# Optimization experiments

Measured on AMD Instinct MI355X. Metric: run time of the kernel, lower is better.

## Reference

```python
import jax, jax.numpy as jnp
import numpy as np
import math

EMBED_DIM = 768
NUM_HEADS = 12
HEAD_DIM = EMBED_DIM // NUM_HEADS
R = 16
LORA_ALPHA = 16
SCALING = LORA_ALPHA / math.sqrt(R)  # 4.0
U = 1.0  # ramp_up_steps=0 -> u()=1.0


def lora_linear(x, W, b, A):
    # base F.linear + SingLoRA delta: delta_W = A @ A.T (symmetric)
    base = x @ W.T + b
    delta_W = A @ A.T  # [D, D]
    return base + (x @ delta_W.T) * (U * SCALING)


def setup_inputs() -> dict:
    key = jax.random.key(0)
    ks = jax.random.split(key, 16)
    B, S, D = 2, 2048, EMBED_DIM
    inv = 1.0 / math.sqrt(D)
    d = {
        'query': jax.random.normal(ks[0], (B, S, D), jnp.float32),
        'key': jax.random.normal(ks[1], (B, S, D), jnp.float32),
        'value': jax.random.normal(ks[2], (B, S, D), jnp.float32),
        'Wq': jax.random.normal(ks[3], (D, D), jnp.float32) * inv,
        'bq': jax.random.normal(ks[4], (D,), jnp.float32) * 0.01,
        'Aq': jax.random.normal(ks[5], (D, R), jnp.float32) * 0.01,
        'Wk': jax.random.normal(ks[6], (D, D), jnp.float32) * inv,
        'bk': jax.random.normal(ks[7], (D,), jnp.float32) * 0.01,
        'Ak': jax.random.normal(ks[8], (D, R), jnp.float32) * 0.01,
        'Wv': jax.random.normal(ks[9], (D, D), jnp.float32) * inv,
        'bv': jax.random.normal(ks[10], (D,), jnp.float32) * 0.01,
        'Av': jax.random.normal(ks[11], (D, R), jnp.float32) * 0.01,
        'Wo': jax.random.normal(ks[12], (D, D), jnp.float32) * inv,
        'bo': jax.random.normal(ks[13], (D,), jnp.float32) * 0.01,
    }
    return d


def reference(query, key, value, Wq, bq, Aq, Wk, bk, Ak, Wv, bv, Av, Wo, bo):
    B, S, D = query.shape
    H, hd = NUM_HEADS, HEAD_DIM
    q = lora_linear(query, Wq, bq, Aq)
    k = lora_linear(key, Wk, bk, Ak)
    v = lora_linear(value, Wv, bv, Av)
    # [B, S, D] -> [B, H, S, hd]
    q = q.reshape(B, S, H, hd).transpose(0, 2, 1, 3)
    k = k.reshape(B, S, H, hd).transpose(0, 2, 1, 3)
    v = v.reshape(B, S, H, hd).transpose(0, 2, 1, 3)
    scores = jnp.einsum('bhqd,bhkd->bhqk', q, k) / math.sqrt(hd)
    attn = jax.nn.softmax(scores, axis=-1)
    out = jnp.einsum('bhqk,bhkd->bhqd', attn, v)  # [B, H, S, hd]
    out = out.transpose(0, 2, 1, 3).reshape(B, S, D)
    out = out @ Wo.T + bo
    return out
```

## Files before the change

### kernel.cpp

```cpp
#include <hip/hip_runtime.h>
#include <math.h>
#include <stdint.h>

#define D 768
#define S 2048
#define B_ 2
#define NROWS 4096
#define H 12
#define HD 64
#define R_ 16

typedef _Float16 half_t;
typedef _Float16 half8 __attribute__((ext_vector_type(8)));
typedef _Float16 half4 __attribute__((ext_vector_type(4)));
typedef float floatx4 __attribute__((ext_vector_type(4)));

#define MFMA32(a, b, c) __builtin_amdgcn_mfma_f32_16x16x32_f16(a, b, c, 0, 0, 0)
#define EXP2F(x) __builtin_amdgcn_exp2f(x)

#define SWAIT(N) __builtin_amdgcn_s_waitcnt(0x0F70 | (N))
#define SBAR() __builtin_amdgcn_s_barrier()

__device__ __forceinline__ void gl_lds16(const void* gp, half_t* lp) {
  __builtin_amdgcn_global_load_lds(
      (const __attribute__((address_space(1))) void*)(gp),
      (__attribute__((address_space(3))) void*)(lp), 16, 0, 0);
}


__global__ __launch_bounds__(256) void prep_kernel(
    const float* __restrict__ q, const float* __restrict__ k,
    const float* __restrict__ v, half_t* __restrict__ xq,
    half_t* __restrict__ xk, half_t* __restrict__ xv,
    const float* __restrict__ Wq, const float* __restrict__ Aq,
    const float* __restrict__ Wk, const float* __restrict__ Ak,
    const float* __restrict__ Wv, const float* __restrict__ Av,
    const float* __restrict__ Wo, half_t* __restrict__ Mq,
    half_t* __restrict__ Mk, half_t* __restrict__ Mv,
    half_t* __restrict__ Mo) {
  const int bid = blockIdx.x;
  if (bid < 9216) {
    const int y = bid / 3072;
    const float* x = (y == 0) ? q : (y == 1) ? k : v;
    half_t* o = (y == 0) ? xq : (y == 1) ? xk : xv;
    int i = (bid - y * 3072) * 1024 + threadIdx.x * 4;
    float4 vv = *reinterpret_cast<const float4*>(x + i);
    half_t tmp[4] = {(half_t)vv.x, (half_t)vv.y, (half_t)vv.z, (half_t)vv.w};
    *reinterpret_cast<uint64_t*>(o + i) = *reinterpret_cast<uint64_t*>(tmp);
  } else {
    const int u = bid - 9216;
    const int y = u / 2304;
    const float* W = (y == 0) ? Wq : (y == 1) ? Wk : (y == 2) ? Wv : Wo;
    const float* A = (y == 0) ? Aq : (y == 1) ? Ak : (y == 2) ? Av : nullptr;
    half_t* M = (y == 0) ? Mq : (y == 1) ? Mk : (y == 2) ? Mv : Mo;
    int idx = (u - y * 2304) * 256 + threadIdx.x;
    int j = idx / D;
    int kk = idx - j * D;
    float acc = W[idx];
    if (A != nullptr) {
      float s = 0.f;
#pragma unroll
      for (int r = 0; r < R_; ++r) s += A[kk * R_ + r] * A[j * R_ + r];
      acc += 4.0f * s;
    }
    M[idx] = (half_t)acc;
  }
}

__global__ __launch_bounds__(256) void gemm_qkv_kernel(
    const half_t* __restrict__ x0, const half_t* __restrict__ x1,
    const half_t* __restrict__ x2, const half_t* __restrict__ m0,
    const half_t* __restrict__ m1, const half_t* __restrict__ m2,
    const float* __restrict__ b0, const float* __restrict__ b1,
    const float* __restrict__ b2, half_t* __restrict__ o0,
    half_t* __restrict__ o1, half_t* __restrict__ o2) {
  constexpr int AG = 8;
  constexpr int G = 16;
  constexpr int PB = G * 512;
  __shared__ __align__(16) half_t smem[3 * PB];

  int lin = blockIdx.x + 6 * (blockIdx.y + 32 * blockIdx.z);
  lin = (lin & 7) * 72 + (lin >> 3);
  const int z = lin / 192;
  const int rem = lin - z * 192;
  const int by = rem / 6;
  const int bx = rem - by * 6;

  const half_t* X = (z == 0) ? x0 : (z == 1) ? x1 : x2;
  const half_t* M = (z == 0) ? m0 : (z == 1) ? m1 : m2;
  const float* bias = (z == 0) ? b0 : (z == 1) ? b1 : b2;
  half_t* Out = (z == 0) ? o0 : (z == 1) ? o1 : o2;

  const int tid = threadIdx.x;
  const int lane = tid & 63;
  const int wv = tid >> 6;
  const int lr = lane & 15;
  const int lq = lane >> 4;
  const int row0 = by * 128;
  const int j0 = bx * 128;
  const int wr = wv >> 1;
  const int wc = wv & 1;

  floatx4 acc[4][4] = {};

#define GSTAGE(soff, k0)                                                      \
  do {                                                                        \
    _Pragma("unroll") for (int gi = 0; gi < 4; ++gi) {                        \
      int g = wv * 4 + gi;                                                    \
      if (g < AG) {                                                           \
        gl_lds16(X + (size_t)(row0 + g * 16 + lr) * D + (k0) + lq * 8,        \
                 smem + (soff) + g * 512);                                    \
      } else {                                                                \
        gl_lds16(M + (size_t)(j0 + (g - AG) * 16 + lr) * D + (k0) + lq * 8,   \
                 smem + (soff) + g * 512);                                    \
      }                                                                       \
    }                                                                         \
  } while (0)

  GSTAGE(0, 0);
  GSTAGE(PB, 32);
  SWAIT(4);
  SBAR();

  int co = 0, so = 2 * PB;
  for (int it = 0; it < D / 32; ++it) {
    if (it + 2 < D / 32) GSTAGE(so, (it + 2) * 32);
    const half_t* Ab = smem + co;
    const half_t* Bb = Ab + AG * 512;
    half8 af[4], bf[4];
#pragma unroll
    for (int t = 0; t < 4; ++t)
      af[t] = *reinterpret_cast<const half8*>(
          &Ab[((wr * 4 + t) * 64 + lane) * 8]);
#pragma unroll
    for (int u = 0; u < 4; ++u)
      bf[u] = *reinterpret_cast<const half8*>(
          &Bb[((wc * 4 + u) * 64 + lane) * 8]);
#pragma unroll
    for (int t = 0; t < 4; ++t)
#pragma unroll
      for (int u = 0; u < 4; ++u) acc[t][u] = MFMA32(af[t], bf[u], acc[t][u]);
    if (it + 2 < D / 32) SWAIT(4); else SWAIT(0);
    SBAR();
    co += PB; if (co == 3 * PB) co = 0;
    so += PB; if (so == 3 * PB) so = 0;
  }
#undef GSTAGE

  float bv[4];
#pragma unroll
  for (int u = 0; u < 4; ++u) bv[u] = bias[j0 + (wc * 4 + u) * 16 + lr];

  if (z == 2) {
    const int bb = row0 >> 11;
    const int kb0 = (row0 & 2047) >> 6;
#pragma unroll
    for (int t = 0; t < 4; ++t) {
#pragma unroll
      for (int u = 0; u < 4; ++u) {
        int gc = j0 + (wc * 4 + u) * 16 + lr;
        int hh = gc >> 6;
        int ud = (gc & 63) >> 4;
        half4 hv;
#pragma unroll
        for (int r = 0; r < 4; ++r) hv[r] = (half_t)(acc[t][u][r] + bv[u]);
        size_t addr = ((size_t)(bb * H + hh) * HD) * S +
                      (size_t)(kb0 + wr) * 4096 +
                      (ud * 2 + ((t >> 1) & 1)) * 512 + lane * 8 + (t & 1) * 4;
        *reinterpret_cast<half4*>(&Out[addr]) = hv;
      }
    }
    return;
  }

#pragma unroll
  for (int t = 0; t < 4; ++t) {
#pragma unroll
    for (int u = 0; u < 4; ++u) {
#pragma unroll
      for (int r = 0; r < 4; ++r) {
        int gr = row0 + (wr * 4 + t) * 16 + lq * 4 + r;
        int gc = j0 + (wc * 4 + u) * 16 + lr;
        Out[(size_t)gr * D + gc] = (half_t)(acc[t][u][r] + bv[u]);
      }
    }
  }
}

__global__ __launch_bounds__(256) void gemm_o_kernel(
    const half_t* __restrict__ Xh, const half_t* __restrict__ M,
    const float* __restrict__ bias, float* __restrict__ Out) {
  constexpr int AG = 8;
  constexpr int G = 16;
  constexpr int PB = G * 512;
  __shared__ __align__(16) half_t smem[3 * PB];

  int lin = blockIdx.x + 12 * blockIdx.y;
  lin = (lin & 7) * 96 + (lin >> 3);
  const int bx = lin % 12;
  const int byy = lin / 12;

  const int tid = threadIdx.x;
  const int lane = tid & 63;
  const int wv = tid >> 6;
  const int lr = lane & 15;
  const int lq = lane >> 4;
  const int row0 = byy * 64;
  const int j0 = bx * 64;
  const int wr = wv >> 1;
  const int wc = wv & 1;

  floatx4 acc[2][2] = {};

#define GSTAGE(soff, k0)                                                       \
  do {                                                                         \
    _Pragma("unroll") for (int gi = 0; gi < 4; ++gi) {                         \
      int g = wv * 4 + gi;                                                     \
      if (g < AG) {                                                            \
        int t = g >> 1, c = g & 1;                                             \
        gl_lds16(                                                              \
            Xh + (size_t)(row0 + t * 16 + lr) * D + (k0) + c * 32 + lq * 8,    \
            smem + (soff) + g * 512);                                          \
      } else {                                                                 \
        int g2 = g - AG;                                                       \
        int u = g2 >> 1, c = g2 & 1;                                           \
        gl_lds16(                                                              \
            M + (size_t)(j0 + u * 16 + lr) * D + (k0) + c * 32 + lq * 8,       \
            smem + (soff) + AG * 512 + g2 * 512);                              \
      }                                                                        \
    }                                                                          \
  } while (0)

  GSTAGE(0, 0);
  GSTAGE(PB, 64);
  SWAIT(4);
  SBAR();

  int co = 0, so = 2 * PB;
  for (int it = 0; it < D / 64; ++it) {
    if (it + 2 < D / 64) GSTAGE(so, (it + 2) * 64);
    const half_t* Ab = smem + co;
    const half_t* Bb = Ab + AG * 512;
#pragma unroll
    for (int c = 0; c < 2; ++c) {
      half8 af[2], bf[2];
#pragma unroll
      for (int t = 0; t < 2; ++t)
        af[t] = *reinterpret_cast<const half8*>(
            &Ab[(((wr * 2 + t) * 2 + c) * 64 + lane) * 8]);
#pragma unroll
      for (int u = 0; u < 2; ++u)
        bf[u] = *reinterpret_cast<const half8*>(
            &Bb[(((wc * 2 + u) * 2 + c) * 64 + lane) * 8]);
#pragma unroll
      for (int t = 0; t < 2; ++t)
#pragma unroll
        for (int u = 0; u < 2; ++u) acc[t][u] = MFMA32(af[t], bf[u], acc[t][u]);
    }
    if (it + 2 < D / 64) SWAIT(4); else SWAIT(0);
    SBAR();
    co += PB; if (co == 3 * PB) co = 0;
    so += PB; if (so == 3 * PB) so = 0;
  }
#undef GSTAGE

  float bv[2];
#pragma unroll
  for (int u = 0; u < 2; ++u) bv[u] = bias[j0 + (wc * 2 + u) * 16 + lr];
#pragma unroll
  for (int t = 0; t < 2; ++t) {
#pragma unroll
    for (int u = 0; u < 2; ++u) {
#pragma unroll
      for (int r = 0; r < 4; ++r) {
        int gr = row0 + (wr * 2 + t) * 16 + lq * 4 + r;
        int gc = j0 + (wc * 2 + u) * 16 + lr;
        Out[(size_t)gr * D + gc] = acc[t][u][r] + bv[u];
      }
    }
  }
}

__global__ __launch_bounds__(512, 6) void attn_mfma_kernel(
    const half_t* __restrict__ Qh, const half_t* __restrict__ Kh,
    const half_t* __restrict__ Vt2, half_t* __restrict__ Oh) {
  __shared__ __align__(16) half_t smem[24576];
  half_t* Ks = smem;
  half_t* Vs = smem + 12288;

  const int tid = threadIdx.x;
  const int lane = tid & 63;
  const int wv = tid >> 6;
  const int t_ = wv & 3;
  const int half_ = wv >> 2;
  const int lr = lane & 15;
  const int lq = lane >> 4;

  int lin = blockIdx.x + 32 * (blockIdx.y + 12 * blockIdx.z);
  lin = (lin & 7) * 96 + (lin >> 3);
  const int q0 = (lin & 31) * 64;
  const int hb = lin >> 5;
  const int h = hb % 12;
  const int b = hb / 12;

  const size_t base = (size_t)b * S * D + h * HD;
  const size_t vtbase = (size_t)(b * H + h) * HD * (size_t)S;
  const int qw = q0 + t_ * 16;

  const half_t qscale = (half_t)0.18033688f;
  half8 qf[2];
#pragma unroll
  for (int c = 0; c < 2; ++c) {
    half8 qv = *reinterpret_cast<const half8*>(
        &Qh[base + (size_t)(qw + lr) * D + c * 32 + lq * 8]);
#pragma unroll
    for (int j = 0; j < 8; ++j) qv[j] = qv[j] * qscale;
    qf[c] = qv;
  }

  half8 ones8;
#pragma unroll
  for (int j = 0; j < 8; ++j) ones8[j] = (half_t)1.0f;

  floatx4 o[4] = {};
  floatx4 ol = {};

#define STAGE(soff, kb)                                                        \
  do {                                                                         \
    _Pragma("unroll") for (int gi = 0; gi < 2; ++gi) {                         \
      int g = wv * 2 + gi;                                                     \
      if (g < 8) {                                                             \
        int u = g >> 1, c = g & 1;                                             \
        gl_lds16(                                                              \
            Kh + base + (size_t)((kb) + u * 16 + lr) * D + c * 32 + lq * 8,    \
            Ks + (soff) + g * 512);                                            \
      } else {                                                                 \
        int gv = g - 8;                                                        \
        gl_lds16(Vt2 + vtbase + (size_t)(kb)*64 + gv * 512 + lane * 8,         \
                 Vs + (soff) + gv * 512);                                      \
      }                                                                        \
    }                                                                          \
  } while (0)

  STAGE(0, 0);
  STAGE(4096, 64);
  SWAIT(2);
  SBAR();

  int co = 0, so = 8192;
  for (int it = 0; it < S / 64; ++it) {
    if (it + 2 < S / 64) STAGE(so, (it + 2) * 64);

    half8 pv;
#pragma unroll
    for (int ui = 0; ui < 2; ++ui) {
      const int u = half_ * 2 + ui;
      half8 kf0 = *reinterpret_cast<const half8*>(
          &Ks[co + ((u * 2 + 0) * 64 + lane) * 8]);
      half8 kf1 = *reinterpret_cast<const half8*>(
          &Ks[co + ((u * 2 + 1) * 64 + lane) * 8]);
      floatx4 st = {};
      st = MFMA32(kf0, qf[0], st);
      st = MFMA32(kf1, qf[1], st);
      pv[4 * ui + 0] = (half_t)EXP2F(st[0]);
      pv[4 * ui + 1] = (half_t)EXP2F(st[1]);
      pv[4 * ui + 2] = (half_t)EXP2F(st[2]);
      pv[4 * ui + 3] = (half_t)EXP2F(st[3]);
    }
#pragma unroll
    for (int ud = 0; ud < 4; ++ud) {
      half8 vf8 = *reinterpret_cast<const half8*>(
          &Vs[co + ((ud * 2 + half_) * 64 + lane) * 8]);
      o[ud] = MFMA32(pv, vf8, o[ud]);
    }
    ol = MFMA32(pv, ones8, ol);

    if (it + 2 < S / 64) SWAIT(2); else SWAIT(0);
    SBAR();
    co += 4096; if (co == 12288) co = 0;
    so += 4096; if (so == 12288) so = 0;
  }
#undef STAGE

  float* red = (float*)smem;
  const int slot = t_ * 64 + lane;
  if (half_ == 1) {
#pragma unroll
    for (int comp = 0; comp < 16; ++comp)
      red[comp * 260 + slot] = o[comp >> 2][comp & 3];
#pragma unroll
    for (int r = 0; r < 4; ++r) red[(16 + r) * 260 + slot] = ol[r];
  }
  __syncthreads();
  if (half_ == 0) {
#pragma unroll
    for (int comp = 0; comp < 16; ++comp)
      o[comp >> 2][comp & 3] += red[comp * 260 + slot];
    float linv[4];
#pragma unroll
    for (int r = 0; r < 4; ++r)
      linv[r] = 1.0f / (ol[r] + red[(16 + r) * 260 + slot]);
#pragma unroll
    for (int ud = 0; ud < 4; ++ud) {
#pragma unroll
      for (int r = 0; r < 4; ++r) {
        int row = qw + lq * 4 + r;
        int col = h * HD + ud * 16 + lr;
        Oh[(size_t)(b * S + row) * D + col] = (half_t)(o[ud][r] * linv[r]);
      }
    }
  }
}

extern "C" void kernel_launch(void* const* d_in, const int* in_sizes, int n_in,
                              void* d_out, int out_size, void* d_ws,
                              size_t ws_size, hipStream_t stream) {
  const float* query = (const float*)d_in[0];
  const float* key   = (const float*)d_in[1];
  const float* value = (const float*)d_in[2];
  const float* Wq = (const float*)d_in[3];
  const float* bq = (const float*)d_in[4];
  const float* Aq = (const float*)d_in[5];
  const float* Wk = (const float*)d_in[6];
  const float* bk = (const float*)d_in[7];
  const float* Ak = (const float*)d_in[8];
  const float* Wv = (const float*)d_in[9];
  const float* bv = (const float*)d_in[10];
  const float* Av = (const float*)d_in[11];
  const float* Wo = (const float*)d_in[12];
  const float* bo = (const float*)d_in[13];
  float* out = (float*)d_out;

  half_t* hw = (half_t*)d_ws;
  const size_t XSZ = (size_t)NROWS * D;
  const size_t MSZ = (size_t)D * D;
  half_t* xq = hw;
  half_t* xk = xq + XSZ;
  half_t* xv = xk + XSZ;
  half_t* qh = xv + XSZ;
  half_t* kh = qh + XSZ;
  half_t* vt = kh + XSZ;
  half_t* ab = vt + XSZ;
  half_t* Mq = ab + XSZ;
  half_t* Mk = Mq + MSZ;
  half_t* Mv = Mk + MSZ;
  half_t* Mo = Mv + MSZ;

  prep_kernel<<<18432, 256, 0, stream>>>(query, key, value, xq, xk, xv, Wq, Aq,
                                         Wk, Ak, Wv, Av, Wo, Mq, Mk, Mv, Mo);

  dim3 gq(D / 128, NROWS / 128, 3);
  gemm_qkv_kernel<<<gq, 256, 0, stream>>>(xq, xk, xv, Mq, Mk, Mv, bq, bk, bv,
                                          qh, kh, vt);

  dim3 ga(S / 64, H, B_);
  attn_mfma_kernel<<<ga, 512, 0, stream>>>(qh, kh, vt, ab);

  dim3 go(D / 64, NROWS / 64, 1);
  gemm_o_kernel<<<go, 256, 0, stream>>>(ab, Mo, bo, out);
}
```

Before: 211.0 us.

## Halve attention block to 4 waves, each handling two query tiles

Each attention block now uses 256 threads instead of 512, and each wave processes two 16-row query tiles. K and V fragments read from LDS are reused across both tiles, which halves LDS read traffic per unit of MFMA work, and each wave issues more global-to-LDS staging loads. s_setprio hints are placed around the MFMA sections so waves in their matrix phase get priority over the others. The cost is higher register pressure from doubled accumulators and fewer waves per block to hide latency.

```diff
diff --git a/kernel.cpp b/kernel.cpp
--- a/kernel.cpp
+++ b/kernel.cpp
@@ -20,6 +20,7 @@
 
 #define SWAIT(N) __builtin_amdgcn_s_waitcnt(0x0F70 | (N))
 #define SBAR() __builtin_amdgcn_s_barrier()
+#define SETPRIO(N) __builtin_amdgcn_s_setprio(N)
 
 __device__ __forceinline__ void gl_lds16(const void* gp, half_t* lp) {
   __builtin_amdgcn_global_load_lds(
@@ -281,7 +282,7 @@
   }
 }
 
-__global__ __launch_bounds__(512, 6) void attn_mfma_kernel(
+__global__ __launch_bounds__(256, 3) void attn_mfma_kernel(
     const half_t* __restrict__ Qh, const half_t* __restrict__ Kh,
     const half_t* __restrict__ Vt2, half_t* __restrict__ Oh) {
   __shared__ __align__(16) half_t smem[24576];
@@ -291,8 +292,8 @@
   const int tid = threadIdx.x;
   const int lane = tid & 63;
   const int wv = tid >> 6;
-  const int t_ = wv & 3;
-  const int half_ = wv >> 2;
+  const int qp = wv >> 1;
+  const int half_ = wv & 1;
   const int lr = lane & 15;
   const int lq = lane >> 4;
 
@@ -305,30 +306,33 @@
 
   const size_t base = (size_t)b * S * D + h * HD;
   const size_t vtbase = (size_t)(b * H + h) * HD * (size_t)S;
-  const int qw = q0 + t_ * 16;
 
   const half_t qscale = (half_t)0.18033688f;
-  half8 qf[2];
-#pragma unroll
-  for (int c = 0; c < 2; ++c) {
-    half8 qv = *reinterpret_cast<const half8*>(
-        &Qh[base + (size_t)(qw + lr) * D + c * 32 + lq * 8]);
-#pragma unroll
-    for (int j = 0; j < 8; ++j) qv[j] = qv[j] * qscale;
-    qf[c] = qv;
+  half8 qf[2][2];
+#pragma unroll
+  for (int s = 0; s < 2; ++s) {
+    const int qw = q0 + (qp * 2 + s) * 16;
+#pragma unroll
+    for (int c = 0; c < 2; ++c) {
+      half8 qv = *reinterpret_cast<const half8*>(
+          &Qh[base + (size_t)(qw + lr) * D + c * 32 + lq * 8]);
+#pragma unroll
+      for (int j = 0; j < 8; ++j) qv[j] = qv[j] * qscale;
+      qf[s][c] = qv;
+    }
   }
 
   half8 ones8;
 #pragma unroll
   for (int j = 0; j < 8; ++j) ones8[j] = (half_t)1.0f;
 
-  floatx4 o[4] = {};
-  floatx4 ol = {};
+  floatx4 o[2][4] = {};
+  floatx4 ol[2] = {};
 
 #define STAGE(soff, kb)                                                        \
   do {                                                                         \
-    _Pragma("unroll") for (int gi = 0; gi < 2; ++gi) {                         \
-      int g = wv * 2 + gi;                                                     \
+    _Pragma("unroll") for (int gi = 0; gi < 4; ++gi) {                         \
+      int g = wv * 4 + gi;                                                     \
       if (g < 8) {                                                             \
         int u = g >> 1, c = g & 1;                                             \
         gl_lds16(                                                              \
@@ -344,14 +348,14 @@
 
   STAGE(0, 0);
   STAGE(4096, 64);
-  SWAIT(2);
+  SWAIT(4);
   SBAR();
 
   int co = 0, so = 8192;
   for (int it = 0; it < S / 64; ++it) {
     if (it + 2 < S / 64) STAGE(so, (it + 2) * 64);
 
-    half8 pv;
+    half8 pv[2];
 #pragma unroll
     for (int ui = 0; ui < 2; ++ui) {
       const int u = half_ * 2 + ui;
@@ -359,23 +363,32 @@
           &Ks[co + ((u * 2 + 0) * 64 + lane) * 8]);
       half8 kf1 = *reinterpret_cast<const half8*>(
           &Ks[co + ((u * 2 + 1) * 64 + lane) * 8]);
-      floatx4 st = {};
-      st = MFMA32(kf0, qf[0], st);
-      st = MFMA32(kf1, qf[1], st);
-      pv[4 * ui + 0] = (half_t)EXP2F(st[0]);
-      pv[4 * ui + 1] = (half_t)EXP2F(st[1]);
-      pv[4 * ui + 2] = (half_t)EXP2F(st[2]);
-      pv[4 * ui + 3] = (half_t)EXP2F(st[3]);
-    }
+      SETPRIO(1);
+      floatx4 st0 = {}, st1 = {};
+      st0 = MFMA32(kf0, qf[0][0], st0);
+      st0 = MFMA32(kf1, qf[0][1], st0);
+      st1 = MFMA32(kf0, qf[1][0], st1);
+      st1 = MFMA32(kf1, qf[1][1], st1);
+      SETPRIO(0);
+#pragma unroll
+      for (int j = 0; j < 4; ++j) {
+        pv[0][4 * ui + j] = (half_t)EXP2F(st0[j]);
+        pv[1][4 * ui + j] = (half_t)EXP2F(st1[j]);
+      }
+    }
+    SETPRIO(1);
 #pragma unroll
     for (int ud = 0; ud < 4; ++ud) {
       half8 vf8 = *reinterpret_cast<const half8*>(
           &Vs[co + ((ud * 2 + half_) * 64 + lane) * 8]);
-      o[ud] = MFMA32(pv, vf8, o[ud]);
-    }
-    ol = MFMA32(pv, ones8, ol);
-
-    if (it + 2 < S / 64) SWAIT(2); else SWAIT(0);
+      o[0][ud] = MFMA32(pv[0], vf8, o[0][ud]);
+      o[1][ud] = MFMA32(pv[1], vf8, o[1][ud]);
+    }
+    ol[0] = MFMA32(pv[0], ones8, ol[0]);
+    ol[1] = MFMA32(pv[1], ones8, ol[1]);
+    SETPRIO(0);
+
+    if (it + 2 < S / 64) SWAIT(4); else SWAIT(0);
     SBAR();
     co += 4096; if (co == 12288) co = 0;
     so += 4096; if (so == 12288) so = 0;
@@ -383,30 +396,36 @@
 #undef STAGE
 
   float* red = (float*)smem;
-  const int slot = t_ * 64 + lane;
   if (half_ == 1) {
 #pragma unroll
-    for (int comp = 0; comp < 16; ++comp)
-      red[comp * 260 + slot] = o[comp >> 2][comp & 3];
-#pragma unroll
-    for (int r = 0; r < 4; ++r) red[(16 + r) * 260 + slot] = ol[r];
+    for (int s = 0; s < 2; ++s) {
+      const int slot = (qp * 2 + s) * 64 + lane;
+#pragma unroll
+      for (int comp = 0; comp < 16; ++comp)
+        red[comp * 260 + slot] = o[s][comp >> 2][comp & 3];
+#pragma unroll
+      for (int r = 0; r < 4; ++r) red[(16 + r) * 260 + slot] = ol[s][r];
+    }
   }
   __syncthreads();
   if (half_ == 0) {
 #pragma unroll
-    for (int comp = 0; comp < 16; ++comp)
-      o[comp >> 2][comp & 3] += red[comp * 260 + slot];
-    float linv[4];
-#pragma unroll
-    for (int r = 0; r < 4; ++r)
-      linv[r] = 1.0f / (ol[r] + red[(16 + r) * 260 + slot]);
-#pragma unroll
-    for (int ud = 0; ud < 4; ++ud) {
-#pragma unroll
-      for (int r = 0; r < 4; ++r) {
-        int row = qw + lq * 4 + r;
-        int col = h * HD + ud * 16 + lr;
-        Oh[(size_t)(b * S + row) * D + col] = (half_t)(o[ud][r] * linv[r]);
+    for (int s = 0; s < 2; ++s) {
+      const int slot = (qp * 2 + s) * 64 + lane;
+      const int qw = q0 + (qp * 2 + s) * 16;
+      float linv[4];
+#pragma unroll
+      for (int r = 0; r < 4; ++r)
+        linv[r] = 1.0f / (ol[s][r] + red[(16 + r) * 260 + slot]);
+#pragma unroll
+      for (int ud = 0; ud < 4; ++ud) {
+#pragma unroll
+        for (int r = 0; r < 4; ++r) {
+          float ov = o[s][ud][r] + red[(ud * 4 + r) * 260 + slot];
+          int row = qw + lq * 4 + r;
+          int col = h * HD + ud * 16 + lr;
+          Oh[(size_t)(b * S + row) * D + col] = (half_t)(ov * linv[r]);
+        }
       }
     }
   }
@@ -454,7 +473,7 @@
                                           qh, kh, vt);
 
   dim3 ga(S / 64, H, B_);
-  attn_mfma_kernel<<<ga, 512, 0, stream>>>(qh, kh, vt, ab);
+  attn_mfma_kernel<<<ga, 256, 0, stream>>>(qh, kh, vt, ab);
 
   dim3 go(D / 64, NROWS / 64, 1);
   gemm_o_kernel<<<go, 256, 0, stream>>>(ab, Mo, bo, out);
```

Result: no change. 210.2 us (-0.4%).
